# Optimization experiments

Measured on AMD Instinct MI355X. Metric: run time of the kernel, lower is better.

Reference implementation:

```python
import jax, jax.numpy as jnp
import numpy as np

TEMPERATURE = 0.1
EPS = 1e-12  # F.normalize eps

B, D = 4096, 1024

def setup_inputs() -> dict:
    key = jax.random.key(0)
    k1, k2 = jax.random.split(key)
    return {
        "feature_view_1": jax.random.normal(k1, (B, D), dtype=jnp.float32),
        "feature_view_2": jax.random.normal(k2, (B, D), dtype=jnp.float32),
    }

def reference(feature_view_1, feature_view_2):
    b = feature_view_1.shape[0]
    n = 2 * b  # n_views = 2
    # cat views and L2-normalize each row (F.normalize semantics: x / max(||x||, eps))
    f = jnp.concatenate([feature_view_1, feature_view_2], axis=0)  # [2B, D]
    norm = jnp.maximum(jnp.linalg.norm(f, axis=1, keepdims=True), EPS)
    f = f / norm
    # similarity matrix scaled by temperature
    sim = jnp.matmul(f, f.T) / TEMPERATURE  # [2B, 2B]
    idx = jnp.arange(n)
    # positive for row i is the other view of the same sample: column (i+B) mod 2B
    pos = sim[idx, (idx + b) % n]  # [2B]
    # cross-entropy with label 0 over [pos, negatives] == lse over off-diagonal minus pos
    sim_offdiag = jnp.where(idx[:, None] == idx[None, :], -jnp.inf, sim)
    lse = jax.nn.logsumexp(sim_offdiag, axis=1)  # [2B]
    # CrossEntropyLoss default reduction: mean
    return jnp.mean(lse - pos)
```

## Files before the change

### kernel.cpp

```cpp
#include <hip/hip_runtime.h>
#include <stdint.h>

#define B_ROWS 4096
#define N_ROWS 8192
#define D_DIM  1024
#define NBLK   64
#define NTRI   2080
#define XCDQ   260

typedef __attribute__((ext_vector_type(8))) short bf16x8;
typedef __attribute__((ext_vector_type(4))) float f32x4;

static __device__ __forceinline__ unsigned short f2bf(float f) {
  uint32_t u = __float_as_uint(f);
  u += 0x7fff + ((u >> 16) & 1);
  return (unsigned short)(u >> 16);
}

static __device__ __forceinline__ void async_copy16(const unsigned short* g, unsigned short* l) {
  __builtin_amdgcn_global_load_lds(
      (const __attribute__((address_space(1))) unsigned int*)g,
      (__attribute__((address_space(3))) unsigned int*)l, 16, 0, 0);
}

static __device__ __forceinline__ void wg_barrier() {
  asm volatile("" ::: "memory");
  __builtin_amdgcn_s_barrier();
  asm volatile("" ::: "memory");
}

__global__ __launch_bounds__(256) void normalize_kernel(
    const float* __restrict__ f1, const float* __restrict__ f2,
    unsigned short* __restrict__ F, float* __restrict__ rowsum) {
  const int row = blockIdx.x;
  const int tid = threadIdx.x;
  const float* src = (row < B_ROWS) ? (f1 + (size_t)row * D_DIM)
                                    : (f2 + (size_t)(row - B_ROWS) * D_DIM);
  float4 v = ((const float4*)src)[tid];
  float ss = v.x * v.x + v.y * v.y + v.z * v.z + v.w * v.w;
#pragma unroll
  for (int m = 1; m < 64; m <<= 1) ss += __shfl_xor(ss, m, 64);
  __shared__ float red[4];
  if ((tid & 63) == 0) red[tid >> 6] = ss;
  __syncthreads();
  ss = red[0] + red[1] + red[2] + red[3];
  const float invn = 1.0f / fmaxf(sqrtf(ss), 1e-12f);
  ushort4 o;
  o.x = f2bf(v.x * invn); o.y = f2bf(v.y * invn);
  o.z = f2bf(v.z * invn); o.w = f2bf(v.w * invn);
  ((ushort4*)(F + (size_t)row * D_DIM))[tid] = o;
  if (tid == 0) rowsum[row] = 0.0f;
}

__global__ __launch_bounds__(256, 3) void simloss_kernel(
    const unsigned short* __restrict__ F, float* __restrict__ rowsum,
    float* __restrict__ pos) {
  __shared__ unsigned short lA[3][128 * 32];
  __shared__ unsigned short lB[3][128 * 32];

  int s = (blockIdx.x & 7) * XCDQ + (blockIdx.x >> 3);
  int SJ = 0;
  for (;;) { const int c = 64 * SJ + 36; if (s < c) break; s -= c; ++SJ; }
  int SI = 0;
  while (SI < SJ && s >= 64) { s -= 64; ++SI; }
  int di, dj;
  if (SI < SJ) {
    dj = s >> 3; di = s & 7;
  } else {
    dj = 0; while (s > dj) { s -= (dj + 1); ++dj; } di = s;
  }
  const int bi = SI * 8 + di;
  const int bj = SJ * 8 + dj;

  const int tid  = threadIdx.x;
  const int lane = tid & 63;
  const int wv   = __builtin_amdgcn_readfirstlane(tid >> 6);
  const int waveRow = wv >> 1;
  const int waveCol = wv & 1;
  const int q   = lane >> 4;
  const int l16 = lane & 15;

  const int iBase = bi * 128;
  const int jBase = bj * 128;
  const unsigned short* __restrict__ GA = F + (size_t)iBase * D_DIM;
  const unsigned short* __restrict__ GB = F + (size_t)jBase * D_DIM;

  f32x4 acc[4][4];
#pragma unroll
  for (int a = 0; a < 4; ++a)
#pragma unroll
    for (int b = 0; b < 4; ++b) acc[a][b] = (f32x4){0.f, 0.f, 0.f, 0.f};

#define STAGE(BUFI, K0)                                                      \
  {                                                                          \
    _Pragma("unroll") for (int it = 0; it < 2; ++it) {                       \
      const int lc = it * 256 + tid;                                         \
      const int r  = lc >> 2;                                                \
      const int gc = (lc & 3) ^ ((r >> 1) & 3);                              \
      const size_t goff = (size_t)r * D_DIM + (K0) + gc * 8;                 \
      async_copy16(GA + goff, &lA[BUFI][lc * 8]);                            \
      async_copy16(GB + goff, &lB[BUFI][lc * 8]);                            \
    }                                                                        \
  }

#define STEP(BUFI)                                                           \
  {                                                                          \
    bf16x8 af[4], bfr[4];                                                    \
    _Pragma("unroll") for (int mi = 0; mi < 4; ++mi) {                       \
      const int r  = waveRow * 64 + mi * 16 + l16;                           \
      const int ch = r * 4 + (q ^ ((r >> 1) & 3));                           \
      af[mi] = *(const bf16x8*)&lA[BUFI][ch * 8];                            \
    }                                                                        \
    _Pragma("unroll") for (int ni = 0; ni < 4; ++ni) {                       \
      const int r  = waveCol * 64 + ni * 16 + l16;                           \
      const int ch = r * 4 + (q ^ ((r >> 1) & 3));                           \
      bfr[ni] = *(const bf16x8*)&lB[BUFI][ch * 8];                           \
    }                                                                        \
    _Pragma("unroll") for (int mi = 0; mi < 4; ++mi)                         \
      _Pragma("unroll") for (int ni = 0; ni < 4; ++ni)                       \
        acc[mi][ni] = __builtin_amdgcn_mfma_f32_16x16x32_bf16(               \
            af[mi], bfr[ni], acc[mi][ni], 0, 0, 0);                          \
  }

  STAGE(0, 0)
  STAGE(1, 32)

#pragma unroll 1
  for (int t = 0; t < 32; ++t) {
    if (t == 31) { asm volatile("s_waitcnt vmcnt(0)" ::: "memory"); }
    else         { asm volatile("s_waitcnt vmcnt(4)" ::: "memory"); }
    wg_barrier();
    if (t < 30) { STAGE((t + 2) % 3, (t + 2) * 32) }
    STEP(t % 3)
  }
#undef STEP
#undef STAGE

  const bool offdiag = (bi != bj);
  float colAcc[4] = {0.f, 0.f, 0.f, 0.f};

#pragma unroll
  for (int mi = 0; mi < 4; ++mi) {
#pragma unroll
    for (int reg = 0; reg < 4; ++reg) {
      const int i = iBase + waveRow * 64 + mi * 16 + q * 4 + reg;
      float s2 = 0.0f;
#pragma unroll
      for (int ni = 0; ni < 4; ++ni) {
        const int j = jBase + waveCol * 64 + ni * 16 + l16;
        const float sim = acc[mi][ni][reg] * 10.0f;
        const float e = (j == i) ? 0.0f : __expf(sim - 10.0f);
        s2 += e;
        colAcc[ni] += e;
        if (i < B_ROWS && j == i + B_ROWS) pos[i] = sim;
      }
#pragma unroll
      for (int m = 1; m < 16; m <<= 1) s2 += __shfl_xor(s2, m, 64);
      if (l16 == 0) atomicAdd(&rowsum[i], s2);
    }
  }

  if (offdiag) {
#pragma unroll
    for (int ni = 0; ni < 4; ++ni) {
      float c = colAcc[ni];
      c += __shfl_xor(c, 16, 64);
      c += __shfl_xor(c, 32, 64);
      if (q == 0) {
        const int j = jBase + waveCol * 64 + ni * 16 + l16;
        atomicAdd(&rowsum[j], c);
      }
    }
  }
}

__global__ __launch_bounds__(1024) void finalize_kernel(
    const float* __restrict__ rowsum, const float* __restrict__ pos,
    float* __restrict__ out) {
  const int tid = threadIdx.x;
  float a = 0.0f;
  for (int i = tid; i < N_ROWS; i += 1024)
    a += logf(rowsum[i]) + 10.0f - pos[i & (B_ROWS - 1)];
#pragma unroll
  for (int m = 1; m < 64; m <<= 1) a += __shfl_xor(a, m, 64);
  __shared__ float red[16];
  if ((tid & 63) == 0) red[tid >> 6] = a;
  __syncthreads();
  if (tid == 0) {
    float t = 0.0f;
#pragma unroll
    for (int w = 0; w < 16; ++w) t += red[w];
    out[0] = t * (1.0f / N_ROWS);
  }
}

extern "C" void kernel_launch(void* const* d_in, const int* in_sizes, int n_in,
                              void* d_out, int out_size, void* d_ws, size_t ws_size,
                              hipStream_t stream) {
  const float* f1 = (const float*)d_in[0];
  const float* f2 = (const float*)d_in[1];
  unsigned short* F = (unsigned short*)d_ws;
  float* rowsum = (float*)((char*)d_ws + (size_t)N_ROWS * D_DIM * 2);
  float* pos    = rowsum + N_ROWS;
  float* out    = (float*)d_out;

  hipLaunchKernelGGL(normalize_kernel, dim3(N_ROWS), dim3(256), 0, stream, f1, f2, F, rowsum);
  hipLaunchKernelGGL(simloss_kernel, dim3(NTRI), dim3(256), 0, stream, F, rowsum, pos);
  hipLaunchKernelGGL(finalize_kernel, dim3(1), dim3(1024), 0, stream, rowsum, pos, out);
}
```

Measured before the change: 172.7 us.

## Widen similarity tiles to 128x256 and remap triangular block schedule

```diff
diff --git a/kernel.cpp b/kernel.cpp
--- a/kernel.cpp
+++ b/kernel.cpp
@@ -4,9 +4,10 @@
 #define B_ROWS 4096
 #define N_ROWS 8192
 #define D_DIM  1024
-#define NBLK   64
-#define NTRI   2080
-#define XCDQ   260
+#define NRB    64
+#define NCB    32
+#define NBLKS  1056
+#define XCDQ   132
 
 typedef __attribute__((ext_vector_type(8))) short bf16x8;
 typedef __attribute__((ext_vector_type(4))) float f32x4;
@@ -52,25 +53,20 @@
   if (tid == 0) rowsum[row] = 0.0f;
 }
 
-__global__ __launch_bounds__(256, 3) void simloss_kernel(
+__global__ __launch_bounds__(256, 2) void simloss_kernel(
     const unsigned short* __restrict__ F, float* __restrict__ rowsum,
     float* __restrict__ pos) {
   __shared__ unsigned short lA[3][128 * 32];
-  __shared__ unsigned short lB[3][128 * 32];
+  __shared__ unsigned short lB[3][256 * 32];
 
   int s = (blockIdx.x & 7) * XCDQ + (blockIdx.x >> 3);
-  int SJ = 0;
-  for (;;) { const int c = 64 * SJ + 36; if (s < c) break; s -= c; ++SJ; }
-  int SI = 0;
-  while (SI < SJ && s >= 64) { s -= 64; ++SI; }
-  int di, dj;
-  if (SI < SJ) {
-    dj = s >> 3; di = s & 7;
-  } else {
-    dj = 0; while (s > dj) { s -= (dj + 1); ++dj; } di = s;
-  }
-  const int bi = SI * 8 + di;
-  const int bj = SJ * 8 + dj;
+  int c = 0;
+  for (;;) {
+    const int nr = (2 * c + 2 < 64) ? 2 * c + 2 : 64;
+    if (s < nr) break;
+    s -= nr; ++c;
+  }
+  const int r = s;
 
   const int tid  = threadIdx.x;
   const int lane = tid & 63;
@@ -80,44 +76,50 @@
   const int q   = lane >> 4;
   const int l16 = lane & 15;
 
-  const int iBase = bi * 128;
-  const int jBase = bj * 128;
+  const int iBase = r * 128;
+  const int jBase = c * 256;
   const unsigned short* __restrict__ GA = F + (size_t)iBase * D_DIM;
   const unsigned short* __restrict__ GB = F + (size_t)jBase * D_DIM;
 
-  f32x4 acc[4][4];
+  f32x4 acc[4][8];
 #pragma unroll
   for (int a = 0; a < 4; ++a)
 #pragma unroll
-    for (int b = 0; b < 4; ++b) acc[a][b] = (f32x4){0.f, 0.f, 0.f, 0.f};
+    for (int b = 0; b < 8; ++b) acc[a][b] = (f32x4){0.f, 0.f, 0.f, 0.f};
 
 #define STAGE(BUFI, K0)                                                      \
   {                                                                          \
     _Pragma("unroll") for (int it = 0; it < 2; ++it) {                       \
       const int lc = it * 256 + tid;                                         \
-      const int r  = lc >> 2;                                                \
-      const int gc = (lc & 3) ^ ((r >> 1) & 3);                              \
-      const size_t goff = (size_t)r * D_DIM + (K0) + gc * 8;                 \
+      const int rr = lc >> 2;                                                \
+      const int gc = (lc & 3) ^ ((rr >> 1) & 3);                             \
+      const size_t goff = (size_t)rr * D_DIM + (K0) + gc * 8;                \
       async_copy16(GA + goff, &lA[BUFI][lc * 8]);                            \
+    }                                                                        \
+    _Pragma("unroll") for (int it = 0; it < 4; ++it) {                       \
+      const int lc = it * 256 + tid;                                         \
+      const int rr = lc >> 2;                                                \
+      const int gc = (lc & 3) ^ ((rr >> 1) & 3);                             \
+      const size_t goff = (size_t)rr * D_DIM + (K0) + gc * 8;                \
       async_copy16(GB + goff, &lB[BUFI][lc * 8]);                            \
     }                                                                        \
   }
 
 #define STEP(BUFI)                                                           \
   {                                                                          \
-    bf16x8 af[4], bfr[4];                                                    \
+    bf16x8 af[4], bfr[8];                                                    \
     _Pragma("unroll") for (int mi = 0; mi < 4; ++mi) {                       \
-      const int r  = waveRow * 64 + mi * 16 + l16;                           \
-      const int ch = r * 4 + (q ^ ((r >> 1) & 3));                           \
+      const int rr = waveRow * 64 + mi * 16 + l16;                           \
+      const int ch = rr * 4 + (q ^ ((rr >> 1) & 3));                         \
       af[mi] = *(const bf16x8*)&lA[BUFI][ch * 8];                            \
     }                                                                        \
-    _Pragma("unroll") for (int ni = 0; ni < 4; ++ni) {                       \
-      const int r  = waveCol * 64 + ni * 16 + l16;                           \
-      const int ch = r * 4 + (q ^ ((r >> 1) & 3));                           \
+    _Pragma("unroll") for (int ni = 0; ni < 8; ++ni) {                       \
+      const int rr = waveCol * 128 + ni * 16 + l16;                          \
+      const int ch = rr * 4 + (q ^ ((rr >> 1) & 3));                         \
       bfr[ni] = *(const bf16x8*)&lB[BUFI][ch * 8];                           \
     }                                                                        \
     _Pragma("unroll") for (int mi = 0; mi < 4; ++mi)                         \
-      _Pragma("unroll") for (int ni = 0; ni < 4; ++ni)                       \
+      _Pragma("unroll") for (int ni = 0; ni < 8; ++ni)                       \
         acc[mi][ni] = __builtin_amdgcn_mfma_f32_16x16x32_bf16(               \
             af[mi], bfr[ni], acc[mi][ni], 0, 0, 0);                          \
   }
@@ -128,7 +130,7 @@
 #pragma unroll 1
   for (int t = 0; t < 32; ++t) {
     if (t == 31) { asm volatile("s_waitcnt vmcnt(0)" ::: "memory"); }
-    else         { asm volatile("s_waitcnt vmcnt(4)" ::: "memory"); }
+    else         { asm volatile("s_waitcnt vmcnt(6)" ::: "memory"); }
     wg_barrier();
     if (t < 30) { STAGE((t + 2) % 3, (t + 2) * 32) }
     STEP(t % 3)
@@ -136,8 +138,7 @@
 #undef STEP
 #undef STAGE
 
-  const bool offdiag = (bi != bj);
-  float colAcc[4] = {0.f, 0.f, 0.f, 0.f};
+  float colAcc[8] = {0.f, 0.f, 0.f, 0.f, 0.f, 0.f, 0.f, 0.f};
 
 #pragma unroll
   for (int mi = 0; mi < 4; ++mi) {
@@ -146,10 +147,10 @@
       const int i = iBase + waveRow * 64 + mi * 16 + q * 4 + reg;
       float s2 = 0.0f;
 #pragma unroll
-      for (int ni = 0; ni < 4; ++ni) {
-        const int j = jBase + waveCol * 64 + ni * 16 + l16;
+      for (int ni = 0; ni < 8; ++ni) {
+        const int j = jBase + waveCol * 128 + ni * 16 + l16;
         const float sim = acc[mi][ni][reg] * 10.0f;
-        const float e = (j == i) ? 0.0f : __expf(sim - 10.0f);
+        const float e = (j > i) ? __expf(sim - 10.0f) : 0.0f;
         s2 += e;
         colAcc[ni] += e;
         if (i < B_ROWS && j == i + B_ROWS) pos[i] = sim;
@@ -160,16 +161,14 @@
     }
   }
 
-  if (offdiag) {
-#pragma unroll
-    for (int ni = 0; ni < 4; ++ni) {
-      float c = colAcc[ni];
-      c += __shfl_xor(c, 16, 64);
-      c += __shfl_xor(c, 32, 64);
-      if (q == 0) {
-        const int j = jBase + waveCol * 64 + ni * 16 + l16;
-        atomicAdd(&rowsum[j], c);
-      }
+#pragma unroll
+  for (int ni = 0; ni < 8; ++ni) {
+    float cs = colAcc[ni];
+    cs += __shfl_xor(cs, 16, 64);
+    cs += __shfl_xor(cs, 32, 64);
+    if (q == 0) {
+      const int j = jBase + waveCol * 128 + ni * 16 + l16;
+      atomicAdd(&rowsum[j], cs);
     }
   }
 }
@@ -205,6 +204,6 @@
   float* out    = (float*)d_out;
 
   hipLaunchKernelGGL(normalize_kernel, dim3(N_ROWS), dim3(256), 0, stream, f1, f2, F, rowsum);
-  hipLaunchKernelGGL(simloss_kernel, dim3(NTRI), dim3(256), 0, stream, F, rowsum, pos);
+  hipLaunchKernelGGL(simloss_kernel, dim3(NBLKS), dim3(256), 0, stream, F, rowsum, pos);
   hipLaunchKernelGGL(finalize_kernel, dim3(1), dim3(1024), 0, stream, rowsum, pos, out);
 }
```

New measurement: 185.4 us. +7.4%, slower.

## Switch normalized features and similarity GEMM from bf16 to fp8 MFMA

Applied to the files above, without the earlier changes.

```diff
diff --git a/kernel.cpp b/kernel.cpp
--- a/kernel.cpp
+++ b/kernel.cpp
@@ -8,16 +8,9 @@
 #define NTRI   2080
 #define XCDQ   260
 
-typedef __attribute__((ext_vector_type(8))) short bf16x8;
 typedef __attribute__((ext_vector_type(4))) float f32x4;
 
-static __device__ __forceinline__ unsigned short f2bf(float f) {
-  uint32_t u = __float_as_uint(f);
-  u += 0x7fff + ((u >> 16) & 1);
-  return (unsigned short)(u >> 16);
-}
-
-static __device__ __forceinline__ void async_copy16(const unsigned short* g, unsigned short* l) {
+static __device__ __forceinline__ void async_copy16(const unsigned char* g, unsigned char* l) {
   __builtin_amdgcn_global_load_lds(
       (const __attribute__((address_space(1))) unsigned int*)g,
       (__attribute__((address_space(3))) unsigned int*)l, 16, 0, 0);
@@ -31,7 +24,7 @@
 
 __global__ __launch_bounds__(256) void normalize_kernel(
     const float* __restrict__ f1, const float* __restrict__ f2,
-    unsigned short* __restrict__ F, float* __restrict__ rowsum) {
+    unsigned char* __restrict__ F8, float* __restrict__ rowsum) {
   const int row = blockIdx.x;
   const int tid = threadIdx.x;
   const float* src = (row < B_ROWS) ? (f1 + (size_t)row * D_DIM)
@@ -44,19 +37,19 @@
   if ((tid & 63) == 0) red[tid >> 6] = ss;
   __syncthreads();
   ss = red[0] + red[1] + red[2] + red[3];
-  const float invn = 1.0f / fmaxf(sqrtf(ss), 1e-12f);
-  ushort4 o;
-  o.x = f2bf(v.x * invn); o.y = f2bf(v.y * invn);
-  o.z = f2bf(v.z * invn); o.w = f2bf(v.w * invn);
-  ((ushort4*)(F + (size_t)row * D_DIM))[tid] = o;
+  const float s16 = 16.0f / fmaxf(sqrtf(ss), 1e-12f);
+  int w = 0;
+  w = __builtin_amdgcn_cvt_pk_fp8_f32(v.x * s16, v.y * s16, w, 0);
+  w = __builtin_amdgcn_cvt_pk_fp8_f32(v.z * s16, v.w * s16, w, 1);
+  ((int*)(F8 + (size_t)row * D_DIM))[tid] = w;
   if (tid == 0) rowsum[row] = 0.0f;
 }
 
 __global__ __launch_bounds__(256, 3) void simloss_kernel(
-    const unsigned short* __restrict__ F, float* __restrict__ rowsum,
+    const unsigned char* __restrict__ F8, float* __restrict__ rowsum,
     float* __restrict__ pos) {
-  __shared__ unsigned short lA[3][128 * 32];
-  __shared__ unsigned short lB[3][128 * 32];
+  __shared__ __align__(16) unsigned char lA[3][128 * 64];
+  __shared__ __align__(16) unsigned char lB[3][128 * 64];
 
   int s = (blockIdx.x & 7) * XCDQ + (blockIdx.x >> 3);
   int SJ = 0;
@@ -82,8 +75,8 @@
 
   const int iBase = bi * 128;
   const int jBase = bj * 128;
-  const unsigned short* __restrict__ GA = F + (size_t)iBase * D_DIM;
-  const unsigned short* __restrict__ GB = F + (size_t)jBase * D_DIM;
+  const unsigned char* __restrict__ GA = F8 + (size_t)iBase * D_DIM;
+  const unsigned char* __restrict__ GB = F8 + (size_t)jBase * D_DIM;
 
   f32x4 acc[4][4];
 #pragma unroll
@@ -95,42 +88,55 @@
   {                                                                          \
     _Pragma("unroll") for (int it = 0; it < 2; ++it) {                       \
       const int lc = it * 256 + tid;                                         \
-      const int r  = lc >> 2;                                                \
-      const int gc = (lc & 3) ^ ((r >> 1) & 3);                              \
-      const size_t goff = (size_t)r * D_DIM + (K0) + gc * 8;                 \
-      async_copy16(GA + goff, &lA[BUFI][lc * 8]);                            \
-      async_copy16(GB + goff, &lB[BUFI][lc * 8]);                            \
+      const int rr = lc >> 2;                                                \
+      const int gc = (lc & 3) ^ ((rr >> 1) & 3);                             \
+      const size_t goff = (size_t)rr * D_DIM + (K0) + gc * 16;               \
+      async_copy16(GA + goff, &lA[BUFI][lc * 16]);                           \
+    }                                                                        \
+    _Pragma("unroll") for (int it = 0; it < 2; ++it) {                       \
+      const int lc = it * 256 + tid;                                         \
+      const int rr = lc >> 2;                                                \
+      const int gc = (lc & 3) ^ ((rr >> 1) & 3);                             \
+      const size_t goff = (size_t)rr * D_DIM + (K0) + gc * 16;               \
+      async_copy16(GB + goff, &lB[BUFI][lc * 16]);                           \
     }                                                                        \
   }
 
 #define STEP(BUFI)                                                           \
   {                                                                          \
-    bf16x8 af[4], bfr[4];                                                    \
+    long aF[4][2], bF[4][2];                                                 \
     _Pragma("unroll") for (int mi = 0; mi < 4; ++mi) {                       \
-      const int r  = waveRow * 64 + mi * 16 + l16;                           \
-      const int ch = r * 4 + (q ^ ((r >> 1) & 3));                           \
-      af[mi] = *(const bf16x8*)&lA[BUFI][ch * 8];                            \
+      const int rr  = waveRow * 64 + mi * 16 + l16;                          \
+      const int swz = (rr >> 1) & 3;                                         \
+      const int base = rr * 64 + ((q & 1) << 3);                             \
+      aF[mi][0] = *(const long*)&lA[BUFI][base + ((((q >> 1)    ) ^ swz) << 4)]; \
+      aF[mi][1] = *(const long*)&lA[BUFI][base + ((((q >> 1) + 2) ^ swz) << 4)]; \
     }                                                                        \
     _Pragma("unroll") for (int ni = 0; ni < 4; ++ni) {                       \
-      const int r  = waveCol * 64 + ni * 16 + l16;                           \
-      const int ch = r * 4 + (q ^ ((r >> 1) & 3));                           \
-      bfr[ni] = *(const bf16x8*)&lB[BUFI][ch * 8];                           \
+      const int rr  = waveCol * 64 + ni * 16 + l16;                          \
+      const int swz = (rr >> 1) & 3;                                         \
+      const int base = rr * 64 + ((q & 1) << 3);                             \
+      bF[ni][0] = *(const long*)&lB[BUFI][base + ((((q >> 1)    ) ^ swz) << 4)]; \
+      bF[ni][1] = *(const long*)&lB[BUFI][base + ((((q >> 1) + 2) ^ swz) << 4)]; \
     }                                                                        \
     _Pragma("unroll") for (int mi = 0; mi < 4; ++mi)                         \
-      _Pragma("unroll") for (int ni = 0; ni < 4; ++ni)                       \
-        acc[mi][ni] = __builtin_amdgcn_mfma_f32_16x16x32_bf16(               \
-            af[mi], bfr[ni], acc[mi][ni], 0, 0, 0);                          \
+      _Pragma("unroll") for (int ni = 0; ni < 4; ++ni) {                     \
+        acc[mi][ni] = __builtin_amdgcn_mfma_f32_16x16x32_fp8_fp8(            \
+            aF[mi][0], bF[ni][0], acc[mi][ni], 0, 0, 0);                     \
+        acc[mi][ni] = __builtin_amdgcn_mfma_f32_16x16x32_fp8_fp8(            \
+            aF[mi][1], bF[ni][1], acc[mi][ni], 0, 0, 0);                     \
+      }                                                                      \
   }
 
   STAGE(0, 0)
-  STAGE(1, 32)
+  STAGE(1, 64)
 
 #pragma unroll 1
-  for (int t = 0; t < 32; ++t) {
-    if (t == 31) { asm volatile("s_waitcnt vmcnt(0)" ::: "memory"); }
+  for (int t = 0; t < 16; ++t) {
+    if (t == 15) { asm volatile("s_waitcnt vmcnt(0)" ::: "memory"); }
     else         { asm volatile("s_waitcnt vmcnt(4)" ::: "memory"); }
     wg_barrier();
-    if (t < 30) { STAGE((t + 2) % 3, (t + 2) * 32) }
+    if (t < 14) { STAGE((t + 2) % 3, (t + 2) * 64) }
     STEP(t % 3)
   }
 #undef STEP
@@ -148,7 +154,7 @@
 #pragma unroll
       for (int ni = 0; ni < 4; ++ni) {
         const int j = jBase + waveCol * 64 + ni * 16 + l16;
-        const float sim = acc[mi][ni][reg] * 10.0f;
+        const float sim = acc[mi][ni][reg] * (10.0f / 256.0f);
         const float e = (j == i) ? 0.0f : __expf(sim - 10.0f);
         s2 += e;
         colAcc[ni] += e;
@@ -199,12 +205,12 @@
                               hipStream_t stream) {
   const float* f1 = (const float*)d_in[0];
   const float* f2 = (const float*)d_in[1];
-  unsigned short* F = (unsigned short*)d_ws;
-  float* rowsum = (float*)((char*)d_ws + (size_t)N_ROWS * D_DIM * 2);
+  unsigned char* F8 = (unsigned char*)d_ws;
+  float* rowsum = (float*)((char*)d_ws + (size_t)N_ROWS * D_DIM);
   float* pos    = rowsum + N_ROWS;
   float* out    = (float*)d_out;
 
-  hipLaunchKernelGGL(normalize_kernel, dim3(N_ROWS), dim3(256), 0, stream, f1, f2, F, rowsum);
-  hipLaunchKernelGGL(simloss_kernel, dim3(NTRI), dim3(256), 0, stream, F, rowsum, pos);
+  hipLaunchKernelGGL(normalize_kernel, dim3(N_ROWS), dim3(256), 0, stream, f1, f2, F8, rowsum);
+  hipLaunchKernelGGL(simloss_kernel, dim3(NTRI), dim3(256), 0, stream, F8, rowsum, pos);
   hipLaunchKernelGGL(finalize_kernel, dim3(1), dim3(1024), 0, stream, rowsum, pos, out);
 }
```

Result: faster. 150.4 us (-12.9%).
